# Performance work log

Hardware: AMD Instinct MI355X
Metric: run time of the kernel (lower is better)

Reference implementation:

```python
import jax, jax.numpy as jnp
from jax import lax
import numpy as np

NUM_CENTROIDS = 1024
RADIUS = 0.5
K = 32
EPS = 1e-5


def _fps(xyz, num_samples):
    """Farthest point sampling. Deterministic start at index 0 (torch uses randint)."""
    B, N, _ = xyz.shape

    def step(carry, _):
        distances, farthest = carry
        centroid = jnp.take_along_axis(xyz, farthest[:, None, None], axis=1)  # [B,1,3]
        d = jnp.sum((xyz - centroid) ** 2, axis=-1)  # [B,N]
        distances = jnp.minimum(distances, d)
        nxt = jnp.argmax(distances, axis=-1).astype(jnp.int32)
        return (distances, nxt), farthest

    init = (jnp.full((B, N), jnp.inf, dtype=xyz.dtype), jnp.zeros((B,), jnp.int32))
    _, idxs = lax.scan(step, init, None, length=num_samples)  # [M,B]
    return jnp.transpose(idxs)  # [B,M]


def _ball_query(xyz, new_xyz):
    """K nearest neighbors within RADIUS; out-of-ball slots fall back to nearest."""
    d2 = (jnp.sum(new_xyz ** 2, -1)[:, :, None] + jnp.sum(xyz ** 2, -1)[:, None, :]
          - 2.0 * jnp.einsum('bmd,bnd->bmn', new_xyz, xyz))
    dist = jnp.sqrt(jnp.maximum(d2, 0.0))  # [B,M,N] cdist
    dist = jnp.where(dist > RADIUS, jnp.inf, dist)
    neg_vals, idx = lax.top_k(-dist, K)  # smallest-K distances
    mask = jnp.isinf(neg_vals)  # outside radius
    idx = jnp.where(mask, idx[:, :, 0:1], idx)
    return idx  # [B,M,K]


def _forward(xyz, features, Ws, bs, gs, bts):
    B, N, _ = xyz.shape
    cidx = lax.stop_gradient(_fps(xyz, NUM_CENTROIDS))  # [B,M] int
    new_xyz = jnp.take_along_axis(xyz, cidx[:, :, None], axis=1)  # [B,M,3]
    gidx = lax.stop_gradient(_ball_query(xyz, new_xyz))  # [B,M,K] int
    flat = gidx.reshape(B, -1)
    gxyz = jnp.take_along_axis(xyz, flat[:, :, None], axis=1).reshape(B, NUM_CENTROIDS, K, 3)
    gxyz = gxyz - new_xyz[:, :, None, :]
    gfeat = jnp.take_along_axis(features, flat[:, :, None], axis=1).reshape(B, NUM_CENTROIDS, K, -1)
    h = jnp.concatenate([gxyz, gfeat], axis=-1)  # [B,M,K,C+3]
    for W, b, g, bt in zip(Ws, bs, gs, bts):
        # 1x1 Conv1d == per-point linear over channels
        h = jnp.einsum('bmkc,oc->bmko', h, W) + b
        # BatchNorm1d in training mode: batch stats over (B*M, K), biased var
        mu = jnp.mean(h, axis=(0, 1, 2))
        var = jnp.var(h, axis=(0, 1, 2))
        h = (h - mu) * lax.rsqrt(var + EPS) * g + bt
        h = jax.nn.gelu(h, approximate=False)  # torch nn.GELU default (exact erf)
    return new_xyz, jnp.max(h, axis=2)  # [B,M,3], [B,M,128]


def setup_inputs() -> dict:
    key = jax.random.key(0)
    ks = jax.random.split(key, 8)
    B, N, C = 8, 8192, 64
    xyz = jax.random.normal(ks[0], (B, N, 3), jnp.float32)
    features = jax.random.normal(ks[1], (B, N, C), jnp.float32)
    chans = [C + 3, 64, 64, 128]
    inp = {"xyz": xyz, "features": features}
    for l in range(3):
        cin, cout = chans[l], chans[l + 1]
        inp[f"W{l + 1}"] = jax.random.normal(ks[2 + l], (cout, cin), jnp.float32) / jnp.float32(np.sqrt(cin))
        inp[f"b{l + 1}"] = jnp.zeros((cout,), jnp.float32)
        inp[f"g{l + 1}"] = jnp.ones((cout,), jnp.float32)
        inp[f"bt{l + 1}"] = jnp.zeros((cout,), jnp.float32)
    return inp


def reference(xyz, features, W1, b1, g1, bt1, W2, b2, g2, bt2, W3, b3, g3, bt3):
    return _forward(xyz, features, (W1, W2, W3), (b1, b2, b3), (g1, g2, g3), (bt1, bt2, bt3))
```

## Files before the change

### kernel.cpp

```cpp
#include <hip/hip_runtime.h>
#include <cstdint>
#include <cstddef>

#define BATCH 8
#define NPTS  8192
#define MCENT 1024
#define KNN   32
#define CFEAT 64
#define EPS_F 1e-5f

#define WS_NEED 73400320ull


__device__ __forceinline__ float erf_fast(float x) {
  float a = fabsf(x);
  float t = __builtin_amdgcn_rcpf(fmaf(0.3275911f, a, 1.0f));
  float p = fmaf(1.061405429f, t, -1.453152027f);
  p = fmaf(p, t, 1.421413741f);
  p = fmaf(p, t, -0.284496736f);
  p = fmaf(p, t, 0.254829592f);
  float e = __expf(-a * a);
  float y = fmaf(-p * t, e, 1.0f);
  return copysignf(y, x);
}
__device__ __forceinline__ float gelu_f(float x) {
  return 0.5f * x * (1.0f + erf_fast(x * 0.70710678118654752440f));
}

template<int CTRL>
__device__ __forceinline__ float dpp_max_step(float v) {
  int s = __builtin_amdgcn_update_dpp(__float_as_int(v), __float_as_int(v),
                                      CTRL, 0xf, 0xf, false);
  return fmaxf(v, __int_as_float(s));
}
__device__ __forceinline__ float wave_max_dpp(float v) {
  v = dpp_max_step<0x111>(v);
  v = dpp_max_step<0x112>(v);
  v = dpp_max_step<0x114>(v);
  v = dpp_max_step<0x118>(v);
  v = dpp_max_step<0x142>(v);
  v = dpp_max_step<0x143>(v);
  return v;
}
template<int CTRL>
__device__ __forceinline__ unsigned long long dpp_min64_step(unsigned long long v) {
  int lo = __builtin_amdgcn_update_dpp((int)(unsigned)(v & 0xffffffffull),
                                       (int)(unsigned)(v & 0xffffffffull),
                                       CTRL, 0xf, 0xf, false);
  int hi = __builtin_amdgcn_update_dpp((int)(unsigned)(v >> 32),
                                       (int)(unsigned)(v >> 32),
                                       CTRL, 0xf, 0xf, false);
  unsigned long long o = (((unsigned long long)(unsigned)hi) << 32) | (unsigned)lo;
  return o < v ? o : v;
}
__device__ __forceinline__ unsigned long long wave_min64_dpp(unsigned long long v) {
  v = dpp_min64_step<0x111>(v);
  v = dpp_min64_step<0x112>(v);
  v = dpp_min64_step<0x114>(v);
  v = dpp_min64_step<0x118>(v);
  v = dpp_min64_step<0x142>(v);
  v = dpp_min64_step<0x143>(v);
  return v;
}

template<int M, int HALF>
__device__ __forceinline__ void tree_step(float* s_, float* q_, int lane) {
  bool up = (lane & M) != 0;
#pragma unroll
  for (int j = 0; j < HALF; ++j) {
    float ks = up ? s_[j+HALF] : s_[j];
    float ds = up ? s_[j]      : s_[j+HALF];
    s_[j] = ks + __shfl_xor(ds, M, 64);
    float kq = up ? q_[j+HALF] : q_[j];
    float dq = up ? q_[j]      : q_[j+HALF];
    q_[j] = kq + __shfl_xor(dq, M, 64);
  }
}
template<int M, int HALF>
__device__ __forceinline__ void ptree_step(float* g_, int kbit) {
  bool up = (kbit & M) != 0;
#pragma unroll
  for (int j = 0; j < HALF; ++j) {
    float kv = up ? g_[j+HALF] : g_[j];
    float dv = up ? g_[j]      : g_[j+HALF];
    g_[j] = fmaxf(kv, __shfl_xor(dv, M, 64));
  }
}

#define FPS_STEPS 64
#define BQCAP 512
__global__ __launch_bounds__(512, 1) void mega_kernel(
    const float* __restrict__ xyz, float* __restrict__ new_xyz,
    float* __restrict__ dist_ws, float* __restrict__ cst, int s0,
    int* __restrict__ gidx, const float* __restrict__ feats,
    const float* __restrict__ W1, const float* __restrict__ b1v,
    float* __restrict__ h1, float* __restrict__ part)
{
  __shared__ float pts[NPTS * 3];
  __shared__ float outb[FPS_STEPS * 3];
  __shared__ unsigned long long keys[2][8];
  __shared__ unsigned long long list[8][BQCAP];
  __shared__ float ls[512], lss[512];
  int blk = blockIdx.x, t = threadIdx.x;

  if (blk < 8) {
    if (s0 >= MCENT) return;
    int b = blk;
    const float* xb = xyz + (size_t)b * NPTS * 3;
    float px[16], py[16], pz[16], dist[16];
    {
      const float4* src = (const float4*)(xb + (size_t)t * 48);
      float4 buf[12];
#pragma unroll
      for (int i = 0; i < 12; ++i) buf[i] = src[i];
      const float* f = (const float*)buf;
#pragma unroll
      for (int i = 0; i < 16; ++i) {
        px[i] = f[i*3+0]; py[i] = f[i*3+1]; pz[i] = f[i*3+2];
      }
      float4* dst = (float4*)(pts + (size_t)t * 48);
#pragma unroll
      for (int i = 0; i < 12; ++i) dst[i] = buf[i];
    }
    float* dw = dist_ws + (size_t)b * NPTS + (size_t)t * 16;
    float cx, cy, cz;
    if (s0 == 0) {
#pragma unroll
      for (int i = 0; i < 16; ++i) dist[i] = __builtin_inff();
      cx = xb[0]; cy = xb[1]; cz = xb[2];
    } else {
      float4 d0 = *(const float4*)(dw + 0);
      float4 d1 = *(const float4*)(dw + 4);
      float4 d2 = *(const float4*)(dw + 8);
      float4 d3 = *(const float4*)(dw + 12);
      dist[0]=d0.x; dist[1]=d0.y; dist[2]=d0.z; dist[3]=d0.w;
      dist[4]=d1.x; dist[5]=d1.y; dist[6]=d1.z; dist[7]=d1.w;
      dist[8]=d2.x; dist[9]=d2.y; dist[10]=d2.z; dist[11]=d2.w;
      dist[12]=d3.x; dist[13]=d3.y; dist[14]=d3.z; dist[15]=d3.w;
      cx = cst[b*3+0]; cy = cst[b*3+1]; cz = cst[b*3+2];
    }
    int lane = t & 63, wv = t >> 6;

    for (int s = 0; s < FPS_STEPS; ++s) {
      if (t == 0) { outb[s*3+0] = cx; outb[s*3+1] = cy; outb[s*3+2] = cz; }
      float bd = -1.0f; int bslot = 0;
#pragma unroll
      for (int i = 0; i < 16; ++i) {
        float dx = __fsub_rn(px[i], cx);
        float dy = __fsub_rn(py[i], cy);
        float dz = __fsub_rn(pz[i], cz);
        float d  = __fadd_rn(__fadd_rn(__fmul_rn(dx,dx), __fmul_rn(dy,dy)), __fmul_rn(dz,dz));
        float nd = fminf(dist[i], d);
        dist[i] = nd;
        if (nd > bd) { bd = nd; bslot = i; }
      }
      float w = wave_max_dpp(bd);
      float wmax = __int_as_float(__builtin_amdgcn_readlane(__float_as_int(w), 63));
      unsigned long long mk = __ballot(bd == wmax);
      int sl = __ffsll((long long)mk) - 1;
      int widx = __builtin_amdgcn_readlane(t * 16 + bslot, sl);
      if (lane == 0)
        keys[s & 1][wv] = (((unsigned long long)__float_as_uint(wmax)) << 32)
                          | (unsigned)(8191 - widx);
      __syncthreads();
      unsigned long long bk = keys[s & 1][0];
#pragma unroll
      for (int w2 = 1; w2 < 8; ++w2) {
        unsigned long long o = keys[s & 1][w2];
        if (o > bk) bk = o;
      }
      int idx = 8191 - (int)(unsigned)(bk & 0xffffffffull);
      cx = pts[idx*3+0]; cy = pts[idx*3+1]; cz = pts[idx*3+2];
    }

    *(float4*)(dw + 0)  = make_float4(dist[0], dist[1], dist[2], dist[3]);
    *(float4*)(dw + 4)  = make_float4(dist[4], dist[5], dist[6], dist[7]);
    *(float4*)(dw + 8)  = make_float4(dist[8], dist[9], dist[10], dist[11]);
    *(float4*)(dw + 12) = make_float4(dist[12], dist[13], dist[14], dist[15]);
    if (t == 0) { cst[b*3+0] = cx; cst[b*3+1] = cy; cst[b*3+2] = cz; }
    __syncthreads();
    float* ob = new_xyz + (size_t)b * MCENT * 3 + (size_t)s0 * 3;
    for (int i = t; i < FPS_STEPS * 3; i += 512) ob[i] = outb[i];

  } else if (blk < 72) {
    int ph = s0 - FPS_STEPS;
    if (ph < 0 || ph >= MCENT) return;
    int wv = t >> 6, lane = t & 63;
    int c  = (blk - 8) * 8 + wv;
    int b  = c >> 6;
    int ci = ph + (c & 63);
    int gm = b * MCENT + ci;
    const float* cc = new_xyz + (size_t)gm * 3;
    float c0 = cc[0], c1 = cc[1], c2 = cc[2];
    float sc = __fadd_rn(__fadd_rn(__fmul_rn(c0,c0), __fmul_rn(c1,c1)), __fmul_rn(c2,c2));
    const float* xb = xyz + (size_t)b * NPTS * 3;

    unsigned cnt = 0;
    for (int j0 = 0; j0 < NPTS; j0 += 64) {
      int j = j0 + lane;
      float x = xb[j*3+0], y = xb[j*3+1], z = xb[j*3+2];
      float sx  = __fadd_rn(__fadd_rn(__fmul_rn(x,x), __fmul_rn(y,y)), __fmul_rn(z,z));
      float dot = __fadd_rn(__fadd_rn(__fmul_rn(c0,x), __fmul_rn(c1,y)), __fmul_rn(c2,z));
      float d2  = __fsub_rn(__fadd_rn(sc, sx), __fmul_rn(2.0f, dot));
      float dist = sqrtf(fmaxf(d2, 0.0f));
      bool in_ = (dist <= 0.5f);
      unsigned long long mask = __ballot(in_);
      unsigned off = (unsigned)__popcll(mask & ((1ull << lane) - 1ull));
      if (in_) {
        unsigned pos = cnt + off;
        if (pos < BQCAP)
          list[wv][pos] = (((unsigned long long)__float_as_uint(dist)) << 32) | (unsigned)j;
      }
      cnt += (unsigned)__popcll(mask);
    }
    if (cnt > BQCAP) cnt = BQCAP;

    unsigned long long e[8];
#pragma unroll
    for (int i = 0; i < 8; ++i) {
      unsigned pos = (unsigned)lane + ((unsigned)i << 6);
      e[i] = (pos < cnt) ? list[wv][pos] : ~0ull;
    }
#define CE_(a_, b_) { bool sw = e[b_] < e[a_]; \
                      unsigned long long lo_ = sw ? e[b_] : e[a_]; \
                      unsigned long long hi_ = sw ? e[a_] : e[b_]; \
                      e[a_] = lo_; e[b_] = hi_; }
    CE_(0,1) CE_(2,3) CE_(4,5) CE_(6,7)
    CE_(0,2) CE_(1,3) CE_(4,6) CE_(5,7)
    CE_(1,2) CE_(5,6)
    CE_(0,4) CE_(1,5) CE_(2,6) CE_(3,7)
    CE_(2,4) CE_(3,5)
    CE_(1,2) CE_(3,4) CE_(5,6)
#undef CE_

    int* gout = gidx + (size_t)gm * KNN;
    int first = 0;
    int kmax = (cnt < (unsigned)KNN) ? (int)cnt : KNN;
    for (int k = 0; k < KNN; ++k) {
      if (k < kmax) {
        unsigned long long wr = wave_min64_dpp(e[0]);
        unsigned lo32 = (unsigned)__builtin_amdgcn_readlane((int)(unsigned)(wr & 0xffffffffull), 63);
        unsigned hi32 = (unsigned)__builtin_amdgcn_readlane((int)(unsigned)(wr >> 32), 63);
        unsigned long long wmin = (((unsigned long long)hi32) << 32) | lo32;
        int idxv = (int)lo32;
        if (k == 0) first = idxv;
        if (lane == 0) gout[k] = idxv;
        bool win = (e[0] == wmin);
#pragma unroll
        for (int i = 0; i < 7; ++i) e[i] = win ? e[i+1] : e[i];
        e[7] = win ? ~0ull : e[7];
      } else {
        if (lane == 0) gout[k] = first;
      }
    }

  } else if (blk < 104) {
    int ph = s0 - 2 * FPS_STEPS;
    if (ph < 0 || ph >= MCENT) return;
    int row = (blk - 72) * 512 + t;
    int c   = row >> 5;
    int k   = row & 31;
    int b   = c >> 6;
    int ci  = ph + (c & 63);
    int p   = b * (MCENT * KNN) + ci * KNN + k;
    int idx = gidx[p];
    const float* cc = new_xyz + (size_t)(b * MCENT + ci) * 3;
    const float* q  = xyz + (size_t)(b * NPTS + idx) * 3;
    float in[67];
    in[0] = q[0] - cc[0];
    in[1] = q[1] - cc[1];
    in[2] = q[2] - cc[2];
    const float* fr = feats + (size_t)(b * NPTS + idx) * CFEAT;
#pragma unroll
    for (int j = 0; j < 64; j += 4) {
      float4 v = *(const float4*)(fr + j);
      in[3+j] = v.x; in[4+j] = v.y; in[5+j] = v.z; in[6+j] = v.w;
    }
    float* orow = h1 + (size_t)p * 64;
    for (int o4 = 0; o4 < 16; ++o4) {
      const float* w0 = W1 + (size_t)(o4 * 4) * 67;
      float a0 = b1v[o4*4+0], a1 = b1v[o4*4+1], a2 = b1v[o4*4+2], a3 = b1v[o4*4+3];
#pragma unroll
      for (int j = 0; j < 67; ++j) {
        float x = in[j];
        a0 = fmaf(x, w0[j],       a0);
        a1 = fmaf(x, w0[67+j],    a1);
        a2 = fmaf(x, w0[134+j],   a2);
        a3 = fmaf(x, w0[201+j],   a3);
      }
      *(float4*)(orow + o4*4) = make_float4(a0, a1, a2, a3);
    }

  } else {
    int ph = s0 - 3 * FPS_STEPS;
    if (ph < 0 || ph >= MCENT) return;
    int sb = blk - 104;
    int b  = sb >> 2;
    int rb = (sb & 3) * 512;
    int c  = t & 63, g = t >> 6;
    size_t base = (size_t)b * (MCENT * KNN) + (size_t)ph * KNN + rb;
    float s = 0.0f, ss = 0.0f;
    for (int r = g; r < 512; r += 8) {
      float v = h1[(base + r) * 64 + c];
      s += v;
      ss = fmaf(v, v, ss);
    }
    ls[t] = s; lss[t] = ss;
    __syncthreads();
    if (g == 0) {
#pragma unroll
      for (int gg = 1; gg < 8; ++gg) { s += ls[gg*64 + c]; ss += lss[gg*64 + c]; }
      int pblk = (ph >> 6) * 32 + sb;
      part[(size_t)pblk * 128 + c]      = s;
      part[(size_t)pblk * 128 + 64 + c] = ss;
    }
  }
}

__global__ __launch_bounds__(256) void l2_kernel(
    float* __restrict__ h, const float* __restrict__ W,
    const float* __restrict__ bv, const float* __restrict__ bnp,
    const float* __restrict__ btp)
{
  int p = blockIdx.x * 256 + threadIdx.x;
  float* row = h + (size_t)p * 64;
  float in[64];
#pragma unroll
  for (int j = 0; j < 64; j += 4) {
    float4 v = *(const float4*)(row + j);
    in[j+0] = gelu_f((v.x - bnp[j+0]) * bnp[64+j+0] + btp[j+0]);
    in[j+1] = gelu_f((v.y - bnp[j+1]) * bnp[64+j+1] + btp[j+1]);
    in[j+2] = gelu_f((v.z - bnp[j+2]) * bnp[64+j+2] + btp[j+2]);
    in[j+3] = gelu_f((v.w - bnp[j+3]) * bnp[64+j+3] + btp[j+3]);
  }
  for (int o4 = 0; o4 < 16; ++o4) {
    const float* w0 = W + (size_t)(o4 * 4) * 64;
    float a0 = bv[o4*4+0], a1 = bv[o4*4+1], a2 = bv[o4*4+2], a3 = bv[o4*4+3];
#pragma unroll
    for (int j = 0; j < 64; ++j) {
      float x = in[j];
      a0 = fmaf(x, w0[j],      a0);
      a1 = fmaf(x, w0[64+j],   a1);
      a2 = fmaf(x, w0[128+j],  a2);
      a3 = fmaf(x, w0[192+j],  a3);
    }
    *(float4*)(row + o4*4) = make_float4(a0, a1, a2, a3);
  }
}

template<int C>
__global__ __launch_bounds__(256) void stats_kernel(const float* __restrict__ h,
                                                    float* __restrict__ part)
{
  constexpr int G = 256 / C;
  int t = threadIdx.x;
  int c = t % C, g = t / C;
  const float* base = h + (size_t)blockIdx.x * 512 * C;
  float s = 0.0f, ss = 0.0f;
  for (int r = g; r < 512; r += G) {
    float v = base[(size_t)r * C + c];
    s += v;
    ss = fmaf(v, v, ss);
  }
  __shared__ float ls[256], lss[256];
  ls[t] = s; lss[t] = ss;
  __syncthreads();
  if (g == 0) {
    for (int gg = 1; gg < G; ++gg) { s += ls[gg*C + c]; ss += lss[gg*C + c]; }
    part[(size_t)blockIdx.x * (2*C) + c]     = s;
    part[(size_t)blockIdx.x * (2*C) + C + c] = ss;
  }
}

template<int C>
__global__ __launch_bounds__(256) void fin_kernel(const float* __restrict__ part,
                                                  const float* __restrict__ gv,
                                                  float* __restrict__ bn)
{
  int c = blockIdx.x, t = threadIdx.x;
  float s = 0.0f, ss = 0.0f;
  for (int b2 = t; b2 < 512; b2 += 256) {
    s  += part[(size_t)b2 * (2*C) + c];
    ss += part[(size_t)b2 * (2*C) + C + c];
  }
  __shared__ float ls[256], lss[256];
  ls[t] = s; lss[t] = ss;
  __syncthreads();
  for (int k = 128; k > 0; k >>= 1) {
    if (t < k) { ls[t] += ls[t+k]; lss[t] += lss[t+k]; }
    __syncthreads();
  }
  if (t == 0) {
    const float inv_n = 1.0f / 262144.0f;
    float mu  = ls[0] * inv_n;
    float var = fmaxf(lss[0] * inv_n - mu * mu, 0.0f);
    bn[c]     = mu;
    bn[C + c] = gv[c] / sqrtf(var + EPS_F);
  }
}

__global__ __launch_bounds__(256) void act_kernel(float* __restrict__ h,
                                                  const float* __restrict__ bnp,
                                                  const float* __restrict__ btp)
{
  int p = blockIdx.x * 256 + threadIdx.x;
  float* row = h + (size_t)p * 64;
#pragma unroll
  for (int j = 0; j < 64; j += 4) {
    float4 v = *(const float4*)(row + j);
    v.x = gelu_f((v.x - bnp[j+0]) * bnp[64+j+0] + btp[j+0]);
    v.y = gelu_f((v.y - bnp[j+1]) * bnp[64+j+1] + btp[j+1]);
    v.z = gelu_f((v.z - bnp[j+2]) * bnp[64+j+2] + btp[j+2]);
    v.w = gelu_f((v.w - bnp[j+3]) * bnp[64+j+3] + btp[j+3]);
    *(float4*)(row + j) = v;
  }
}

__global__ __launch_bounds__(256, 1) void l3stats_kernel(
    const float* __restrict__ g2, const float* __restrict__ W3,
    const float* __restrict__ b3, float* __restrict__ part)
{
  int t = threadIdx.x;
  int gb = blockIdx.x >> 2, chunk = blockIdx.x & 3;
  int og0 = chunk * 32;
  int p = gb * 256 + t;
  const float* row = g2 + (size_t)p * 64;
  float in[64];
#pragma unroll
  for (int j = 0; j < 64; j += 4) {
    float4 v = *(const float4*)(row + j);
    in[j+0] = v.x; in[j+1] = v.y; in[j+2] = v.z; in[j+3] = v.w;
  }
  float s_[32], q_[32];
  for (int o4 = 0; o4 < 8; ++o4) {
    const float* w0 = W3 + (size_t)(og0 + o4 * 4) * 64;
    float a0 = b3[og0+o4*4+0], a1 = b3[og0+o4*4+1], a2 = b3[og0+o4*4+2], a3 = b3[og0+o4*4+3];
#pragma unroll
    for (int j = 0; j < 64; ++j) {
      float x = in[j];
      a0 = fmaf(x, w0[j],      a0);
      a1 = fmaf(x, w0[64+j],   a1);
      a2 = fmaf(x, w0[128+j],  a2);
      a3 = fmaf(x, w0[192+j],  a3);
    }
    int o = o4 * 4;
    s_[o]=a0; s_[o+1]=a1; s_[o+2]=a2; s_[o+3]=a3;
    q_[o]=a0*a0; q_[o+1]=a1*a1; q_[o+2]=a2*a2; q_[o+3]=a3*a3;
  }

  int wv = t >> 6, lane = t & 63;
  tree_step<1,16>(s_, q_, lane);
  tree_step<2, 8>(s_, q_, lane);
  tree_step<4, 4>(s_, q_, lane);
  tree_step<8, 2>(s_, q_, lane);
  tree_step<16,1>(s_, q_, lane);
  s_[0] += __shfl_xor(s_[0], 32, 64);
  q_[0] += __shfl_xor(q_[0], 32, 64);

  int ch = (int)(__brev((unsigned)(lane & 31)) >> 27);
  float* pw = part + ((size_t)blockIdx.x * 4 + wv) * 64;
  if (lane < 32) { pw[ch] = s_[0]; pw[32 + ch] = q_[0]; }
}

__global__ __launch_bounds__(256) void fin3_kernel(const float* __restrict__ part,
                                                   const float* __restrict__ gv,
                                                   float* __restrict__ bn)
{
  int c = blockIdx.x, t = threadIdx.x;
  int chunk = c >> 5, j = c & 31;
  float s = 0.0f, ss = 0.0f;
  for (int gb = t; gb < 1024; gb += 256) {
    int blk = gb * 4 + chunk;
#pragma unroll
    for (int wv = 0; wv < 4; ++wv) {
      const float* pw = part + ((size_t)blk * 4 + wv) * 64;
      s  += pw[j];
      ss += pw[32 + j];
    }
  }
  __shared__ float ls[256], lss[256];
  ls[t] = s; lss[t] = ss;
  __syncthreads();
  for (int k = 128; k > 0; k >>= 1) {
    if (t < k) { ls[t] += ls[t+k]; lss[t] += lss[t+k]; }
    __syncthreads();
  }
  if (t == 0) {
    const float inv_n = 1.0f / 262144.0f;
    float mu  = ls[0] * inv_n;
    float var = fmaxf(lss[0] * inv_n - mu * mu, 0.0f);
    bn[c]       = mu;
    bn[128 + c] = gv[c] / sqrtf(var + EPS_F);
  }
}

__global__ __launch_bounds__(256, 1) void pool3_kernel(
    const float* __restrict__ g2, const float* __restrict__ W3,
    const float* __restrict__ b3,
    const float* __restrict__ bnp3,
    const float* __restrict__ btp3,
    float* __restrict__ out1)
{
  int t = threadIdx.x;
  int gb = blockIdx.x >> 2, chunk = blockIdx.x & 3;
  int og0 = chunk * 32;
  int p = gb * 256 + t;
  const float* row = g2 + (size_t)p * 64;
  float in[64];
#pragma unroll
  for (int j = 0; j < 64; j += 4) {
    float4 v = *(const float4*)(row + j);
    in[j+0] = v.x; in[j+1] = v.y; in[j+2] = v.z; in[j+3] = v.w;
  }
  float g_[32];
  for (int o4 = 0; o4 < 8; ++o4) {
    const float* w0 = W3 + (size_t)(og0 + o4 * 4) * 64;
    float a0 = b3[og0+o4*4+0], a1 = b3[og0+o4*4+1], a2 = b3[og0+o4*4+2], a3 = b3[og0+o4*4+3];
#pragma unroll
    for (int j = 0; j < 64; ++j) {
      float x = in[j];
      a0 = fmaf(x, w0[j],      a0);
      a1 = fmaf(x, w0[64+j],   a1);
      a2 = fmaf(x, w0[128+j],  a2);
      a3 = fmaf(x, w0[192+j],  a3);
    }
    int oc0 = og0 + o4 * 4, o = o4 * 4;
    g_[o]   = gelu_f((a0 - bnp3[oc0+0]) * bnp3[128+oc0+0] + btp3[oc0+0]);
    g_[o+1] = gelu_f((a1 - bnp3[oc0+1]) * bnp3[128+oc0+1] + btp3[oc0+1]);
    g_[o+2] = gelu_f((a2 - bnp3[oc0+2]) * bnp3[128+oc0+2] + btp3[oc0+2]);
    g_[o+3] = gelu_f((a3 - bnp3[oc0+3]) * bnp3[128+oc0+3] + btp3[oc0+3]);
  }

  ptree_step<1,16>(g_, t);
  ptree_step<2, 8>(g_, t);
  ptree_step<4, 4>(g_, t);
  ptree_step<8, 2>(g_, t);
  ptree_step<16,1>(g_, t);

  int ch = (int)(__brev((unsigned)(t & 31)) >> 27);
  int gm = gb * 8 + (t >> 5);
  out1[(size_t)gm * 128 + og0 + ch] = g_[0];
}

__global__ void fill_kernel(float* __restrict__ out1) {
  out1[blockIdx.x * 256 + threadIdx.x] = 1.0e6f;
}

extern "C" void kernel_launch(void* const* d_in, const int* in_sizes, int n_in,
                              void* d_out, int out_size, void* d_ws, size_t ws_size,
                              hipStream_t stream)
{
  (void)in_sizes; (void)n_in; (void)out_size;
  const float* xyz   = (const float*)d_in[0];
  const float* feats = (const float*)d_in[1];
  const float* W1  = (const float*)d_in[2];
  const float* b1  = (const float*)d_in[3];
  const float* g1  = (const float*)d_in[4];
  const float* bt1 = (const float*)d_in[5];
  const float* W2  = (const float*)d_in[6];
  const float* b2  = (const float*)d_in[7];
  const float* g2  = (const float*)d_in[8];
  const float* bt2 = (const float*)d_in[9];
  const float* W3  = (const float*)d_in[10];
  const float* b3  = (const float*)d_in[11];
  const float* g3  = (const float*)d_in[12];
  const float* bt3 = (const float*)d_in[13];

  float* out0 = (float*)d_out;
  float* out1 = out0 + (size_t)BATCH * MCENT * 3;

  char* ws = (char*)d_ws;
  int*   gidx    = (int*)(ws + 0);
  float* part    = (float*)(ws + (1u << 20));
  float* bn0     = (float*)(ws + 5u * (1u << 20));
  float* bn1     = bn0 + 128;
  float* bn2     = bn0 + 256;
  float* dist_ws = (float*)(ws + 5u * (1u << 20) + 65536u);
  float* cst     = (float*)(ws + 5u * (1u << 20) + 65536u + 262144u);
  float* h1      = (float*)(ws + 6u * (1u << 20));

  if (ws_size < WS_NEED) {
    fill_kernel<<<4096, 256, 0, stream>>>(out1);
    return;
  }

  for (int s0 = 0; s0 <= MCENT + 2 * FPS_STEPS; s0 += FPS_STEPS)
    mega_kernel<<<136, 512, 0, stream>>>(xyz, out0, dist_ws, cst, s0,
                                         gidx, feats, W1, b1, h1, part);

  fin_kernel<64><<<64, 256, 0, stream>>>(part, g1, bn0);
  l2_kernel<<<1024, 256, 0, stream>>>(h1, W2, b2, bn0, bt1);
  stats_kernel<64><<<512, 256, 0, stream>>>(h1, part);
  fin_kernel<64><<<64, 256, 0, stream>>>(part, g2, bn1);
  act_kernel<<<1024, 256, 0, stream>>>(h1, bn1, bt2);
  l3stats_kernel<<<4096, 256, 0, stream>>>(h1, W3, b3, part);
  fin3_kernel<<<128, 256, 0, stream>>>(part, g3, bn2);
  pool3_kernel<<<4096, 256, 0, stream>>>(h1, W3, b3, bn2, bt3, out1);
}
```

Baseline: 1.505 ms.

## Store layer-3 pre-activations in fp16 to skip recomputing the final matmul

Folds the layer-2 BN+GELU activation into the layer-3 stats kernel and has it write the layer-3 pre-activations to a transposed fp16 buffer in workspace. A new pooling kernel then reads that buffer, applies BN+GELU and takes the max over K, instead of recomputing the 64x128 matmul. This removes the separate act pass and the second matmul, at the cost of about 64 MB of extra fp16 writes and reads, lower precision in the pooled values, and a larger workspace requirement. The old path is kept as a fallback when the workspace is smaller.

After: 1.416 ms. -5.9%, faster.

```diff
diff --git a/kernel.cpp b/kernel.cpp
--- a/kernel.cpp
+++ b/kernel.cpp
@@ -1,4 +1,5 @@
 #include <hip/hip_runtime.h>
+#include <hip/hip_fp16.h>
 #include <cstdint>
 #include <cstddef>
 
@@ -9,7 +10,8 @@
 #define CFEAT 64
 #define EPS_F 1e-5f
 
-#define WS_NEED 73400320ull
+#define WS_NEED_SMALL 73400320ull
+#define WS_NEED_BIG   140509184ull
 
 
 __device__ __forceinline__ float erf_fast(float x) {
@@ -462,6 +464,63 @@
   if (lane < 32) { pw[ch] = s_[0]; pw[32 + ch] = q_[0]; }
 }
 
+__global__ __launch_bounds__(256, 1) void l3stats_h3_kernel(
+    const float* __restrict__ h1, const float* __restrict__ W3,
+    const float* __restrict__ b3, const float* __restrict__ bnp2,
+    const float* __restrict__ btp2, float* __restrict__ part,
+    __half* __restrict__ h3t)
+{
+  int t = threadIdx.x;
+  int gb = blockIdx.x >> 2, chunk = blockIdx.x & 3;
+  int og0 = chunk * 32;
+  int p = gb * 256 + t;
+  const float* row = h1 + (size_t)p * 64;
+  float in[64];
+#pragma unroll
+  for (int j = 0; j < 64; j += 4) {
+    float4 v = *(const float4*)(row + j);
+    in[j+0] = gelu_f((v.x - bnp2[j+0]) * bnp2[64+j+0] + btp2[j+0]);
+    in[j+1] = gelu_f((v.y - bnp2[j+1]) * bnp2[64+j+1] + btp2[j+1]);
+    in[j+2] = gelu_f((v.z - bnp2[j+2]) * bnp2[64+j+2] + btp2[j+2]);
+    in[j+3] = gelu_f((v.w - bnp2[j+3]) * bnp2[64+j+3] + btp2[j+3]);
+  }
+  int gm = p >> 5, kk = p & 31;
+  __half* hb = h3t + ((size_t)gm * 128 + og0) * 32 + kk;
+  float s_[32], q_[32];
+  for (int o4 = 0; o4 < 8; ++o4) {
+    const float* w0 = W3 + (size_t)(og0 + o4 * 4) * 64;
+    float a0 = b3[og0+o4*4+0], a1 = b3[og0+o4*4+1], a2 = b3[og0+o4*4+2], a3 = b3[og0+o4*4+3];
+#pragma unroll
+    for (int j = 0; j < 64; ++j) {
+      float x = in[j];
+      a0 = fmaf(x, w0[j],      a0);
+      a1 = fmaf(x, w0[64+j],   a1);
+      a2 = fmaf(x, w0[128+j],  a2);
+      a3 = fmaf(x, w0[192+j],  a3);
+    }
+    int o = o4 * 4;
+    hb[(size_t)(o+0)*32] = __float2half_rn(a0);
+    hb[(size_t)(o+1)*32] = __float2half_rn(a1);
+    hb[(size_t)(o+2)*32] = __float2half_rn(a2);
+    hb[(size_t)(o+3)*32] = __float2half_rn(a3);
+    s_[o]=a0; s_[o+1]=a1; s_[o+2]=a2; s_[o+3]=a3;
+    q_[o]=a0*a0; q_[o+1]=a1*a1; q_[o+2]=a2*a2; q_[o+3]=a3*a3;
+  }
+
+  int wv = t >> 6, lane = t & 63;
+  tree_step<1,16>(s_, q_, lane);
+  tree_step<2, 8>(s_, q_, lane);
+  tree_step<4, 4>(s_, q_, lane);
+  tree_step<8, 2>(s_, q_, lane);
+  tree_step<16,1>(s_, q_, lane);
+  s_[0] += __shfl_xor(s_[0], 32, 64);
+  q_[0] += __shfl_xor(q_[0], 32, 64);
+
+  int ch = (int)(__brev((unsigned)(lane & 31)) >> 27);
+  float* pw = part + ((size_t)blockIdx.x * 4 + wv) * 64;
+  if (lane < 32) { pw[ch] = s_[0]; pw[32 + ch] = q_[0]; }
+}
+
 __global__ __launch_bounds__(256) void fin3_kernel(const float* __restrict__ part,
                                                    const float* __restrict__ gv,
                                                    float* __restrict__ bn)
@@ -540,6 +599,32 @@
   int ch = (int)(__brev((unsigned)(t & 31)) >> 27);
   int gm = gb * 8 + (t >> 5);
   out1[(size_t)gm * 128 + og0 + ch] = g_[0];
+}
+
+__global__ __launch_bounds__(256) void pool3t_kernel(
+    const __half* __restrict__ h3t,
+    const float* __restrict__ bnp3, const float* __restrict__ btp3,
+    float* __restrict__ out1)
+{
+  int u = blockIdx.x * 256 + threadIdx.x;
+  int gm = u >> 7, oc = u & 127;
+  float mu = bnp3[oc], a = bnp3[128 + oc], bt = btp3[oc];
+  const uint4* src = (const uint4*)(h3t + ((size_t)gm * 128 + oc) * 32);
+  float mx = -__builtin_inff();
+#pragma unroll
+  for (int i = 0; i < 4; ++i) {
+    uint4 v = src[i];
+    unsigned wds[4] = {v.x, v.y, v.z, v.w};
+#pragma unroll
+    for (int w2 = 0; w2 < 4; ++w2) {
+      __half2 hp = *reinterpret_cast<const __half2*>(&wds[w2]);
+      float2 f = __half22float2(hp);
+      float x0 = gelu_f((f.x - mu) * a + bt);
+      float x1 = gelu_f((f.y - mu) * a + bt);
+      mx = fmaxf(mx, fmaxf(x0, x1));
+    }
+  }
+  out1[u] = mx;
 }
 
 __global__ void fill_kernel(float* __restrict__ out1) {
@@ -578,8 +663,9 @@
   float* dist_ws = (float*)(ws + 5u * (1u << 20) + 65536u);
   float* cst     = (float*)(ws + 5u * (1u << 20) + 65536u + 262144u);
   float* h1      = (float*)(ws + 6u * (1u << 20));
-
-  if (ws_size < WS_NEED) {
+  __half* h3t    = (__half*)(ws + 70u * (1u << 20));
+
+  if (ws_size < WS_NEED_SMALL) {
     fill_kernel<<<4096, 256, 0, stream>>>(out1);
     return;
   }
@@ -592,8 +678,15 @@
   l2_kernel<<<1024, 256, 0, stream>>>(h1, W2, b2, bn0, bt1);
   stats_kernel<64><<<512, 256, 0, stream>>>(h1, part);
   fin_kernel<64><<<64, 256, 0, stream>>>(part, g2, bn1);
-  act_kernel<<<1024, 256, 0, stream>>>(h1, bn1, bt2);
-  l3stats_kernel<<<4096, 256, 0, stream>>>(h1, W3, b3, part);
-  fin3_kernel<<<128, 256, 0, stream>>>(part, g3, bn2);
-  pool3_kernel<<<4096, 256, 0, stream>>>(h1, W3, b3, bn2, bt3, out1);
-}
+
+  if (ws_size >= WS_NEED_BIG) {
+    l3stats_h3_kernel<<<4096, 256, 0, stream>>>(h1, W3, b3, bn1, bt2, part, h3t);
+    fin3_kernel<<<128, 256, 0, stream>>>(part, g3, bn2);
+    pool3t_kernel<<<4096, 256, 0, stream>>>(h3t, bn2, bt3, out1);
+  } else {
+    act_kernel<<<1024, 256, 0, stream>>>(h1, bn1, bt2);
+    l3stats_kernel<<<4096, 256, 0, stream>>>(h1, W3, b3, part);
+    fin3_kernel<<<128, 256, 0, stream>>>(part, g3, bn2);
+    pool3_kernel<<<4096, 256, 0, stream>>>(h1, W3, b3, bn2, bt3, out1);
+  }
+}
```
